# Performance work log

Measured on AMD Instinct MI355X. Metric: run time of the kernel, lower is better.

Reference implementation:

```python
import jax, jax.numpy as jnp
import numpy as np
from jax.scipy.special import logsumexp

T, N, M = 131072, 64, 8  # T_max, n_states, m_dimensions


def setup_inputs() -> dict:
    key = jax.random.key(0)
    k1, k2, k3, k4 = jax.random.split(key, 4)
    # observed Poisson counts, shape (T, M)
    x = jax.random.randint(k1, (T, M), 0, 20, dtype=jnp.int32)
    # Poisson rates per state/dimension (positive), shape (N, M)
    lambdas = jnp.exp(jax.random.uniform(k2, (N, M), dtype=jnp.float32) * 3.0)
    # column-stochastic transition matrix in log domain (softmax over dim 0, as in torch code)
    log_transition = jax.nn.log_softmax(
        jax.random.uniform(k3, (N, N), dtype=jnp.float32) * 10.0, axis=0)
    # log state priors, shape (N,)
    log_state_priors = jax.nn.log_softmax(
        jax.random.normal(k4, (N,), dtype=jnp.float32), axis=0)
    return {"x": x, "lambdas": lambdas, "log_transition": log_transition,
            "log_state_priors": log_state_priors}


def reference(x, lambdas, log_transition, log_state_priors):
    """log p(x) for a Poisson-emission HMM (forward algorithm in log domain)."""
    xf = x.astype(jnp.float32)                      # (T, M)
    log_lam = jnp.log(lambdas)                      # (N, M)
    # Poisson log-prob summed over dims: em[t,s] = sum_m x[t,m]*log lam[s,m] - lam[s,m] - lgamma(x[t,m]+1)
    log_em = (xf @ log_lam.T                        # (T, N)
              - lambdas.sum(axis=1)[None, :]
              - jax.lax.lgamma(xf + 1.0).sum(axis=1)[:, None])

    alpha0 = log_em[0] + log_state_priors           # (N,)

    def step(alpha_prev, em_t):
        # alpha[t,i] = em[t,i] + logsumexp_k (A[i,k] + alpha[t-1,k])
        alpha = em_t + logsumexp(log_transition + alpha_prev[None, :], axis=1)
        return alpha, None

    alpha_T, _ = jax.lax.scan(step, alpha0, log_em[1:])
    return logsumexp(alpha_T)
```

## Files before the change

### kernel.cpp

```cpp
#include <hip/hip_runtime.h>
#include <stdint.h>

#define TT 131072
#define MD 8
#define CHUNK 32
#define RMP 72

using f32x4  = __attribute__((ext_vector_type(4))) float;
using bf16x8 = __attribute__((ext_vector_type(8))) __bf16;
using bf16x2 = __attribute__((ext_vector_type(2))) __bf16;
using u32x2  = __attribute__((ext_vector_type(2))) uint32_t;
using u32x4  = __attribute__((ext_vector_type(4))) uint32_t;

__device__ __constant__ float c_lg[20] = {
    0.0f, 0.0f, 0.69314718f, 1.79175947f, 3.17805383f,
    4.78749174f, 6.57925121f, 8.52516136f, 10.60460290f, 12.80182748f,
    15.10441257f, 17.50230785f, 19.98721386f, 22.55216385f, 25.19122118f,
    27.89927138f, 30.67186011f, 33.50507345f, 36.39544521f, 39.33988419f};

#define MFMA(a, b, c) __builtin_amdgcn_mfma_f32_16x16x32_bf16((a), (b), (c), 0, 0, 0)

__device__ __forceinline__ uint32_t pk2(float lo, float hi) {
    bf16x2 t = {(__bf16)lo, (__bf16)hi};
    return __builtin_bit_cast(uint32_t, t);
}

__device__ __forceinline__ float wave_max_dpp(float v) {
    int x = __builtin_bit_cast(int, v);
#define DHOP(ctrl)                                                            \
    {                                                                         \
        int y = __builtin_amdgcn_update_dpp(x, x, ctrl, 0xf, 0xf, false);     \
        x = __builtin_bit_cast(int, fmaxf(__builtin_bit_cast(float, x),       \
                                          __builtin_bit_cast(float, y)));     \
    }
    DHOP(0x111)
    DHOP(0x112)
    DHOP(0x114)
    DHOP(0x118)
    DHOP(0x142)
    DHOP(0x143)
#undef DHOP
    return __builtin_bit_cast(float, __builtin_amdgcn_readlane(x, 63));
}


__device__ __forceinline__ void emis(const int4& xa, const int4& xb,
                                     const float* ll, float lamsum,
                                     const float* lgt, float& pe, float& gs) {
    float g = -lamsum;
    g = fmaf((float)xa.x, ll[0], g);
    g = fmaf((float)xa.y, ll[1], g);
    g = fmaf((float)xa.z, ll[2], g);
    g = fmaf((float)xa.w, ll[3], g);
    g = fmaf((float)xb.x, ll[4], g);
    g = fmaf((float)xb.y, ll[5], g);
    g = fmaf((float)xb.z, ll[6], g);
    g = fmaf((float)xb.w, ll[7], g);
    float Lt = lgt[xa.x] + lgt[xa.y] + lgt[xa.z] + lgt[xa.w] +
               lgt[xb.x] + lgt[xb.y] + lgt[xb.z] + lgt[xb.w];
    float gm = wave_max_dpp(g);
    pe = __expf(g - gm);
    gs = gm - Lt;
}

__device__ __forceinline__ void emis_ng(const int4& xa, const int4& xb,
                                        const float* ll, float lamsum,
                                        float& pe, float& gm_out) {
    float g = -lamsum;
    g = fmaf((float)xa.x, ll[0], g);
    g = fmaf((float)xa.y, ll[1], g);
    g = fmaf((float)xa.z, ll[2], g);
    g = fmaf((float)xa.w, ll[3], g);
    g = fmaf((float)xb.x, ll[4], g);
    g = fmaf((float)xb.y, ll[5], g);
    g = fmaf((float)xb.z, ll[6], g);
    g = fmaf((float)xb.w, ll[7], g);
    float gm = wave_max_dpp(g);
    pe = __expf(g - gm);
    gm_out = gm;
}


__device__ __forceinline__ void identity_B(bf16x8 B[2][4], int li, int q) {
#pragma unroll
    for (int kf = 0; kf < 2; ++kf)
#pragma unroll
        for (int nb = 0; nb < 4; ++nb) {
            int n = 16 * nb + li;
            u32x4 u;
#pragma unroll
            for (int wi = 0; wi < 4; ++wi) {
                int k0 = 32 * kf + 16 * (wi >> 1) + 4 * q + 2 * (wi & 1);
                uint32_t v = 0;
                if (k0 == n) v |= 0x3F80u;
                if (k0 + 1 == n) v |= 0x3F800000u;
                u[wi] = v;
            }
            B[kf][nb] = __builtin_bit_cast(bf16x8, u);
        }
}

__device__ __forceinline__ void state_to_rm(short* rm, const bf16x8 B[2][4],
                                            int li, int q) {
#pragma unroll
    for (int kf = 0; kf < 2; ++kf)
#pragma unroll
        for (int nb = 0; nb < 4; ++nb) {
            u32x4 u = __builtin_bit_cast(u32x4, B[kf][nb]);
            int n = 16 * nb + li;
#pragma unroll
            for (int wi = 0; wi < 4; ++wi) {
                int k0 = 32 * kf + 16 * (wi >> 1) + 4 * q + 2 * (wi & 1);
                uint32_t v = u[wi];
                rm[k0 * RMP + n] = (short)(v & 0xFFFFu);
                rm[(k0 + 1) * RMP + n] = (short)(v >> 16);
            }
        }
}

__device__ __forceinline__ void dump_rm_g(short* gm, const bf16x8 B[2][4],
                                          int li, int q) {
#pragma unroll
    for (int kf = 0; kf < 2; ++kf)
#pragma unroll
        for (int nb = 0; nb < 4; ++nb) {
            u32x4 u = __builtin_bit_cast(u32x4, B[kf][nb]);
            int n = 16 * nb + li;
#pragma unroll
            for (int wi = 0; wi < 4; ++wi) {
                int k0 = 32 * kf + 16 * (wi >> 1) + 4 * q + 2 * (wi & 1);
                uint32_t v = u[wi];
                gm[k0 * 64 + n] = (short)(v & 0xFFFFu);
                gm[(k0 + 1) * 64 + n] = (short)(v >> 16);
            }
        }
}

__device__ __forceinline__ void load_afrags(const short* rm, int li, int q,
                                            bf16x8 A[4][2]) {
#pragma unroll
    for (int mb = 0; mb < 4; ++mb)
#pragma unroll
        for (int kf = 0; kf < 2; ++kf) {
            const short* p = rm + (16 * mb + li) * RMP + 32 * kf + 4 * q;
            u32x2 lo = *(const u32x2*)p;
            u32x2 hi = *(const u32x2*)(p + 16);
            u32x4 u = {lo[0], lo[1], hi[0], hi[1]};
            A[mb][kf] = __builtin_bit_cast(bf16x8, u);
        }
}

__device__ __forceinline__ void load_afrags_g(const short* gm, int li, int q,
                                              bf16x8 A[4][2]) {
#pragma unroll
    for (int mb = 0; mb < 4; ++mb)
#pragma unroll
        for (int kf = 0; kf < 2; ++kf) {
            const short* p = gm + (16 * mb + li) * 64 + 32 * kf + 4 * q;
            u32x2 lo = *(const u32x2*)p;
            u32x2 hi = *(const u32x2*)(p + 16);
            u32x4 u = {lo[0], lo[1], hi[0], hi[1]};
            A[mb][kf] = __builtin_bit_cast(bf16x8, u);
        }
}

__device__ __forceinline__ float leftmul(const bf16x8 A[4][2], bf16x8 B[2][4]) {
    f32x4 d[4][4];
#pragma unroll
    for (int mb = 0; mb < 4; ++mb)
#pragma unroll
        for (int nb = 0; nb < 4; ++nb) {
            f32x4 z = {0.f, 0.f, 0.f, 0.f};
            d[mb][nb] = MFMA(A[mb][0], B[0][nb], z);
            d[mb][nb] = MFMA(A[mb][1], B[1][nb], d[mb][nb]);
        }
    float pm = 0.f;
#pragma unroll
    for (int mb = 0; mb < 4; ++mb)
#pragma unroll
        for (int nb = 0; nb < 4; ++nb)
            pm = fmaxf(pm, fmaxf(fmaxf(d[mb][nb][0], d[mb][nb][1]),
                                 fmaxf(d[mb][nb][2], d[mb][nb][3])));
    pm = wave_max_dpp(pm);
    pm = fmaxf(pm, 1e-30f);
    float r = 1.0f / pm;
#pragma unroll
    for (int mb = 0; mb < 4; ++mb)
#pragma unroll
        for (int nb = 0; nb < 4; ++nb) {
#pragma unroll
            for (int reg = 0; reg < 4; ++reg)
                B[mb >> 1][nb][(mb & 1) * 4 + reg] =
                    (__bf16)(d[mb][nb][reg] * r);
        }
    return pm;
}

#define STEPE(BIN, BOUT, NRM, GSC, GSN, SACC, CHI)                           \
    {                                                                        \
        int sl_ = s + 2 > CHUNK - 1 ? CHUNK - 1 : s + 2;                     \
        int4 xa_ = xs[w][CHI * 64 + 2 * sl_];                                \
        int4 xb_ = xs[w][CHI * 64 + 2 * sl_ + 1];                            \
        float pen_, gmn_;                                                    \
        emis_ng(xa_, xb_, ll, lamsum, pen_, gmn_);                           \
        GSN = gmn_;                                                          \
        pes[(s + 2) & 3][CHI][w][l] = pen_;                                  \
        float r_ = 1.0f / NRM;                                               \
        SACC += (double)GSC + (double)__logf(NRM);                           \
        const float* pc_ = &pes[s & 3][CHI][w][0];                           \
        f32x4 scv0 = *(const f32x4*)(pc_ + 4 * q) * r_;                      \
        f32x4 scv1 = *(const f32x4*)(pc_ + 16 + 4 * q) * r_;                 \
        f32x4 scv2 = *(const f32x4*)(pc_ + 32 + 4 * q) * r_;                 \
        f32x4 scv3 = *(const f32x4*)(pc_ + 48 + 4 * q) * r_;                 \
        f32x4 mx_ = {0.f, 0.f, 0.f, 0.f};                                    \
        _Pragma("unroll") for (int nb = 0; nb < 4; ++nb) {                   \
            f32x4 z = {0.f, 0.f, 0.f, 0.f};                                  \
            f32x4 d0 = MFMA(TA[0][0], BIN[0][nb], z);                        \
            d0 = MFMA(TA[0][1], BIN[1][nb], d0);                             \
            f32x4 d1 = MFMA(TA[1][0], BIN[0][nb], z);                        \
            d1 = MFMA(TA[1][1], BIN[1][nb], d1);                             \
            d0 *= scv0;                                                      \
            d1 *= scv1;                                                      \
            mx_ = __builtin_elementwise_max(mx_, d0);                        \
            mx_ = __builtin_elementwise_max(mx_, d1);                        \
            u32x4 u0 = {pk2(d0[0], d0[1]), pk2(d0[2], d0[3]),                \
                        pk2(d1[0], d1[1]), pk2(d1[2], d1[3])};               \
            BOUT[0][nb] = __builtin_bit_cast(bf16x8, u0);                    \
            f32x4 d2 = MFMA(TA[2][0], BIN[0][nb], z);                        \
            d2 = MFMA(TA[2][1], BIN[1][nb], d2);                             \
            f32x4 d3 = MFMA(TA[3][0], BIN[0][nb], z);                        \
            d3 = MFMA(TA[3][1], BIN[1][nb], d3);                             \
            d2 *= scv2;                                                      \
            d3 *= scv3;                                                      \
            mx_ = __builtin_elementwise_max(mx_, d2);                        \
            mx_ = __builtin_elementwise_max(mx_, d3);                        \
            u32x4 u1 = {pk2(d2[0], d2[1]), pk2(d2[2], d2[3]),                \
                        pk2(d3[0], d3[1]), pk2(d3[2], d3[3])};               \
            BOUT[1][nb] = __builtin_bit_cast(bf16x8, u1);                    \
        }                                                                    \
        float pm_ = fmaxf(fmaxf(mx_[0], mx_[1]), fmaxf(mx_[2], mx_[3]));     \
        pm_ = wave_max_dpp(pm_);                                             \
        NRM = fmaxf(pm_, 1e-30f);                                            \
    }

#define STEPO(BIN, BOUT, GSC, GSN, SACC, CHI)                                \
    {                                                                        \
        int sl_ = s + 2 > CHUNK - 1 ? CHUNK - 1 : s + 2;                     \
        int4 xa_ = xs[w][CHI * 64 + 2 * sl_];                                \
        int4 xb_ = xs[w][CHI * 64 + 2 * sl_ + 1];                            \
        float pen_, gmn_;                                                    \
        emis_ng(xa_, xb_, ll, lamsum, pen_, gmn_);                           \
        GSN = gmn_;                                                          \
        pes[(s + 2) & 3][CHI][w][l] = pen_;                                  \
        SACC += (double)GSC;                                                 \
        const float* pc_ = &pes[s & 3][CHI][w][0];                           \
        f32x4 scv0 = *(const f32x4*)(pc_ + 4 * q);                           \
        f32x4 scv1 = *(const f32x4*)(pc_ + 16 + 4 * q);                      \
        f32x4 scv2 = *(const f32x4*)(pc_ + 32 + 4 * q);                      \
        f32x4 scv3 = *(const f32x4*)(pc_ + 48 + 4 * q);                      \
        _Pragma("unroll") for (int nb = 0; nb < 4; ++nb) {                   \
            f32x4 z = {0.f, 0.f, 0.f, 0.f};                                  \
            f32x4 d0 = MFMA(TA[0][0], BIN[0][nb], z);                        \
            d0 = MFMA(TA[0][1], BIN[1][nb], d0);                             \
            f32x4 d1 = MFMA(TA[1][0], BIN[0][nb], z);                        \
            d1 = MFMA(TA[1][1], BIN[1][nb], d1);                             \
            d0 *= scv0;                                                      \
            d1 *= scv1;                                                      \
            u32x4 u0 = {pk2(d0[0], d0[1]), pk2(d0[2], d0[3]),                \
                        pk2(d1[0], d1[1]), pk2(d1[2], d1[3])};               \
            BOUT[0][nb] = __builtin_bit_cast(bf16x8, u0);                    \
            f32x4 d2 = MFMA(TA[2][0], BIN[0][nb], z);                        \
            d2 = MFMA(TA[2][1], BIN[1][nb], d2);                             \
            f32x4 d3 = MFMA(TA[3][0], BIN[0][nb], z);                        \
            d3 = MFMA(TA[3][1], BIN[1][nb], d3);                             \
            d2 *= scv2;                                                      \
            d3 *= scv3;                                                      \
            u32x4 u1 = {pk2(d2[0], d2[1]), pk2(d2[2], d2[3]),                \
                        pk2(d3[0], d3[1]), pk2(d3[2], d3[3])};               \
            BOUT[1][nb] = __builtin_bit_cast(bf16x8, u1);                    \
        }                                                                    \
        XAUNUSED                                                             \
    }
#define XAUNUSED

__global__ __launch_bounds__(256, 2) void k_chunks(
    const int* __restrict__ x, const float* __restrict__ lambdas,
    const float* __restrict__ logT, short* __restrict__ M1,
    double* __restrict__ S1) {
    __shared__ short rm[4][64 * RMP];
    __shared__ float pes[4][2][4][64];
    __shared__ int4 xs[4][128];
    __shared__ float lgt[20];
    __shared__ double Sw[4];
    const int tid = threadIdx.x;
    const int l = tid & 63, w = tid >> 6;
    const int li = l & 15, q = l >> 4;
    if (tid < 20) lgt[tid] = c_lg[tid];

    const int c0 = (blockIdx.x * 4 + w) * 2;
    const int t0a = 1 + c0 * CHUNK;
    const int t0b = t0a + CHUNK;
    const int lenB = min(CHUNK, TT - t0b);

    {
        int r0 = l >> 1, h = l & 1;
        int tr0 = t0a + r0;
        tr0 = tr0 > TT - 1 ? TT - 1 : tr0;
        xs[w][l] = *(const int4*)(x + (size_t)tr0 * MD + h * 4);
        int tr1 = t0a + 32 + r0;
        tr1 = tr1 > TT - 1 ? TT - 1 : tr1;
        xs[w][l + 64] = *(const int4*)(x + (size_t)tr1 * MD + h * 4);
    }

    float ll[8];
    float lamsum = 0.f;
#pragma unroll
    for (int m = 0; m < 8; ++m) {
        float lam = lambdas[l * 8 + m];
        ll[m] = __logf(lam);
        lamsum += lam;
    }

    bf16x8 TA[4][2];
#pragma unroll
    for (int mb = 0; mb < 4; ++mb)
#pragma unroll
        for (int kf = 0; kf < 2; ++kf) {
            const float* tp = logT + (16 * mb + li) * 64 + 32 * kf + 4 * q;
            float4 v0 = *(const float4*)tp;
            float4 v1 = *(const float4*)(tp + 16);
            bf16x8 a;
            a[0] = (__bf16)__expf(v0.x);
            a[1] = (__bf16)__expf(v0.y);
            a[2] = (__bf16)__expf(v0.z);
            a[3] = (__bf16)__expf(v0.w);
            a[4] = (__bf16)__expf(v1.x);
            a[5] = (__bf16)__expf(v1.y);
            a[6] = (__bf16)__expf(v1.z);
            a[7] = (__bf16)__expf(v1.w);
            TA[mb][kf] = a;
        }

    bf16x8 B0a[2][4], B1a[2][4], B0b[2][4], B1b[2][4];
    identity_B(B0a, li, q);
    identity_B(B0b, li, q);
    __syncthreads();

    double Sa = 0.0, Sb = 0.0;
    float nA_a = 1.0f, nA_b = 1.0f;
    float gE0a, gE1a, gO0a, gO1a;
    float gE0b, gE1b, gO0b, gO1b;
    {
        float pe_;
        emis_ng(xs[w][0], xs[w][1], ll, lamsum, pe_, gE0a);
        pes[0][0][w][l] = pe_;
        emis_ng(xs[w][2], xs[w][3], ll, lamsum, pe_, gO0a);
        pes[1][0][w][l] = pe_;
        emis_ng(xs[w][64], xs[w][65], ll, lamsum, pe_, gE0b);
        pes[0][1][w][l] = pe_;
        emis_ng(xs[w][66], xs[w][67], ll, lamsum, pe_, gO0b);
        pes[1][1][w][l] = pe_;
    }

    int s = 0;
#pragma unroll 1
    for (int p = 0; p < 7; ++p) {
        STEPE(B0a, B1a, nA_a, gE0a, gE1a, Sa, 0);
        STEPE(B0b, B1b, nA_b, gE0b, gE1b, Sb, 1);
        ++s;
        STEPO(B1a, B0a, gO0a, gO1a, Sa, 0);
        STEPO(B1b, B0b, gO0b, gO1b, Sb, 1);
        ++s;
        STEPE(B0a, B1a, nA_a, gE1a, gE0a, Sa, 0);
        STEPE(B0b, B1b, nA_b, gE1b, gE0b, Sb, 1);
        ++s;
        STEPO(B1a, B0a, gO1a, gO0a, Sa, 0);
        STEPO(B1b, B0b, gO1b, gO0b, Sb, 1);
        ++s;
    }
    STEPE(B0a, B1a, nA_a, gE0a, gE1a, Sa, 0);
    STEPE(B0b, B1b, nA_b, gE0b, gE1b, Sb, 1);
    ++s;
    STEPO(B1a, B0a, gO0a, gO1a, Sa, 0);
    STEPO(B1b, B0b, gO0b, gO1b, Sb, 1);
    ++s;
    STEPE(B0a, B1a, nA_a, gE1a, gE0a, Sa, 0);
    STEPE(B0b, B1b, nA_b, gE1b, gE0b, Sb, 1);
    ++s;
    STEPO(B1a, B0a, gO1a, gO0a, Sa, 0);
    if (lenB == CHUNK) {
        STEPO(B1b, B0b, gO1b, gO0b, Sb, 1);
    } else {
#pragma unroll
        for (int kf = 0; kf < 2; ++kf)
#pragma unroll
            for (int nb = 0; nb < 4; ++nb) B0b[kf][nb] = B1b[kf][nb];
    }

    {
        const int lenTot = CHUNK + lenB;
        float lt = 0.f;
        if (l < lenTot) {
            int4 a = xs[w][2 * l], b = xs[w][2 * l + 1];
            lt = lgt[a.x] + lgt[a.y] + lgt[a.z] + lgt[a.w] + lgt[b.x] +
                 lgt[b.y] + lgt[b.z] + lgt[b.w];
        }
#pragma unroll
        for (int m = 1; m <= 32; m <<= 1) lt += __shfl_xor(lt, m, 64);
        Sa -= (double)lt;
    }

    state_to_rm(&rm[w][0], B0b, li, q);
    {
        bf16x8 Ap[4][2];
        load_afrags(&rm[w][0], li, q, Ap);
        float pm = leftmul(Ap, B0a);
        Sa += Sb + (double)__logf(pm);
    }

    __syncthreads();
    if (w) state_to_rm(&rm[w][0], B0a, li, q);
    if (l == 0) Sw[w] = Sa;
    __syncthreads();
    if (w == 0) {
        double S = Sa;
#pragma unroll 1
        for (int j = 1; j < 4; ++j) {
            bf16x8 A[4][2];
            load_afrags(&rm[j][0], li, q, A);
            float pm = leftmul(A, B0a);
            S += Sw[j] + (double)__logf(pm);
        }
        dump_rm_g(M1 + (size_t)blockIdx.x * 4096, B0a, li, q);
        if (l == 0) S1[blockIdx.x] = S;
    }
}

__global__ __launch_bounds__(256, 1) void k_combine(
    const short* __restrict__ M1, const double* __restrict__ S1,
    short* __restrict__ M2, double* __restrict__ S2) {
    __shared__ short rm[4][64 * RMP];
    __shared__ double Sw[4];
    const int tid = threadIdx.x;
    const int l = tid & 63, w = tid >> 6;
    const int li = l & 15, q = l >> 4;
    const int base = (blockIdx.x * 4 + w) * 4;

    bf16x8 B[2][4];
    identity_B(B, li, q);
    double S = 0.0;
    bf16x8 Aa[4][2], Ab[4][2];
    load_afrags_g(M1 + (size_t)base * 4096, li, q, Aa);
    load_afrags_g(M1 + (size_t)(base + 1) * 4096, li, q, Ab);
    float pm = leftmul(Aa, B);
    S += S1[base] + (double)__logf(pm);
    load_afrags_g(M1 + (size_t)(base + 2) * 4096, li, q, Aa);
    pm = leftmul(Ab, B);
    S += S1[base + 1] + (double)__logf(pm);
    load_afrags_g(M1 + (size_t)(base + 3) * 4096, li, q, Ab);
    pm = leftmul(Aa, B);
    S += S1[base + 2] + (double)__logf(pm);
    pm = leftmul(Ab, B);
    S += S1[base + 3] + (double)__logf(pm);

    if (w) state_to_rm(&rm[w][0], B, li, q);
    if (l == 0) Sw[w] = S;
    __syncthreads();
    if (w == 0) {
#pragma unroll 1
        for (int j = 1; j < 4; ++j) {
            bf16x8 A[4][2];
            load_afrags(&rm[j][0], li, q, A);
            float pmj = leftmul(A, B);
            S += Sw[j] + (double)__logf(pmj);
        }
        dump_rm_g(M2 + (size_t)blockIdx.x * 4096, B, li, q);
        if (l == 0) S2[blockIdx.x] = S;
    }
}

__global__ __launch_bounds__(256, 1) void k_final(
    const int* __restrict__ x, const float* __restrict__ lambdas,
    const float* __restrict__ prior, const short* __restrict__ M2,
    const double* __restrict__ S2, float* __restrict__ out) {
    __shared__ short rm[4][64 * RMP];
    __shared__ double Sw[4];
    __shared__ float lgt[20];
    const int tid = threadIdx.x;
    const int l = tid & 63, w = tid >> 6;
    const int li = l & 15, q = l >> 4;
    if (tid < 20) lgt[tid] = c_lg[tid];
    __syncthreads();

    const int base = w * 8;
    bf16x8 B[2][4];
    identity_B(B, li, q);
    double S = 0.0;
    bf16x8 Aa[4][2], Ab[4][2];
    load_afrags_g(M2 + (size_t)base * 4096, li, q, Aa);
#pragma unroll
    for (int j = 0; j < 8; j += 2) {
        load_afrags_g(M2 + (size_t)(base + j + 1) * 4096, li, q, Ab);
        float pm = leftmul(Aa, B);
        S += S2[base + j] + (double)__logf(pm);
        if (j + 2 < 8)
            load_afrags_g(M2 + (size_t)(base + j + 2) * 4096, li, q, Aa);
        pm = leftmul(Ab, B);
        S += S2[base + j + 1] + (double)__logf(pm);
    }

    if (w) state_to_rm(&rm[w][0], B, li, q);
    if (l == 0) Sw[w] = S;
    __syncthreads();
    if (w == 0) {
#pragma unroll 1
        for (int j = 1; j < 4; ++j) {
            bf16x8 A[4][2];
            load_afrags(&rm[j][0], li, q, A);
            float pm = leftmul(A, B);
            S += Sw[j] + (double)__logf(pm);
        }
        float ll[8];
        float lamsum = 0.f;
#pragma unroll
        for (int m = 0; m < 8; ++m) {
            float lam = lambdas[l * 8 + m];
            ll[m] = __logf(lam);
            lamsum += lam;
        }
        int4 xa = *(const int4*)(x);
        int4 xb = *(const int4*)(x + 4);
        float pe0, gs0;
        emis(xa, xb, ll, lamsum, lgt, pe0, gs0);
        S += (double)gs0;
        float a0 = pe0 * __expf(prior[l]);

        float av[4];
#pragma unroll
        for (int nb = 0; nb < 4; ++nb) av[nb] = __shfl(a0, 16 * nb + li, 64);

        float acc = 0.f;
#pragma unroll
        for (int kf = 0; kf < 2; ++kf)
#pragma unroll
            for (int nb = 0; nb < 4; ++nb) {
                u32x4 u = __builtin_bit_cast(u32x4, B[kf][nb]);
#pragma unroll
                for (int e = 0; e < 4; ++e) {
                    float flo = __builtin_bit_cast(float, u[e] << 16);
                    float fhi = __builtin_bit_cast(float, u[e] & 0xFFFF0000u);
                    acc = fmaf(flo + fhi, av[nb], acc);
                }
            }
#pragma unroll
        for (int m = 1; m <= 32; m <<= 1) acc += __shfl_xor(acc, m, 64);
        if (l == 0) out[0] = (float)(S + (double)__logf(acc));
    }
}

extern "C" void kernel_launch(void* const* d_in, const int* in_sizes, int n_in,
                              void* d_out, int out_size, void* d_ws,
                              size_t ws_size, hipStream_t stream) {
    const int* x = (const int*)d_in[0];
    const float* lambdas = (const float*)d_in[1];
    const float* logT = (const float*)d_in[2];
    const float* prior = (const float*)d_in[3];
    float* out = (float*)d_out;
    char* ws = (char*)d_ws;
    short* M1 = (short*)ws;
    double* S1 = (double*)(ws + 4194304);
    short* M2 = (short*)(ws + 4198400);
    double* S2 = (double*)(ws + 4460544);

    k_chunks<<<512, 256, 0, stream>>>(x, lambdas, logT, M1, S1);
    k_combine<<<32, 256, 0, stream>>>(M1, S1, M2, S2);
    k_final<<<1, 256, 0, stream>>>(x, lambdas, prior, M2, S2, out);
}
```

Baseline: 115.1 us.

## Halve chunk length, alias scratch onto rm LDS, double chunk-level parallelism

```diff
diff --git a/kernel.cpp b/kernel.cpp
--- a/kernel.cpp
+++ b/kernel.cpp
@@ -3,7 +3,7 @@
 
 #define TT 131072
 #define MD 8
-#define CHUNK 32
+#define CHUNK 16
 #define RMP 72
 
 using f32x4  = __attribute__((ext_vector_type(4))) float;
@@ -199,15 +199,15 @@
 #define STEPE(BIN, BOUT, NRM, GSC, GSN, SACC, CHI)                           \
     {                                                                        \
         int sl_ = s + 2 > CHUNK - 1 ? CHUNK - 1 : s + 2;                     \
-        int4 xa_ = xs[w][CHI * 64 + 2 * sl_];                                \
-        int4 xb_ = xs[w][CHI * 64 + 2 * sl_ + 1];                            \
+        int4 xa_ = xw[CHI * 32 + 2 * sl_];                                   \
+        int4 xb_ = xw[CHI * 32 + 2 * sl_ + 1];                               \
         float pen_, gmn_;                                                    \
         emis_ng(xa_, xb_, ll, lamsum, pen_, gmn_);                           \
         GSN = gmn_;                                                          \
-        pes[(s + 2) & 3][CHI][w][l] = pen_;                                  \
+        pesf[(((s + 2) & 3) * 8 + CHI * 4 + w) * 64 + l] = pen_;             \
         float r_ = 1.0f / NRM;                                               \
         SACC += (double)GSC + (double)__logf(NRM);                           \
-        const float* pc_ = &pes[s & 3][CHI][w][0];                           \
+        const float* pc_ = pesf + ((s & 3) * 8 + CHI * 4 + w) * 64;          \
         f32x4 scv0 = *(const f32x4*)(pc_ + 4 * q) * r_;                      \
         f32x4 scv1 = *(const f32x4*)(pc_ + 16 + 4 * q) * r_;                 \
         f32x4 scv2 = *(const f32x4*)(pc_ + 32 + 4 * q) * r_;                 \
@@ -246,14 +246,14 @@
 #define STEPO(BIN, BOUT, GSC, GSN, SACC, CHI)                                \
     {                                                                        \
         int sl_ = s + 2 > CHUNK - 1 ? CHUNK - 1 : s + 2;                     \
-        int4 xa_ = xs[w][CHI * 64 + 2 * sl_];                                \
-        int4 xb_ = xs[w][CHI * 64 + 2 * sl_ + 1];                            \
+        int4 xa_ = xw[CHI * 32 + 2 * sl_];                                   \
+        int4 xb_ = xw[CHI * 32 + 2 * sl_ + 1];                               \
         float pen_, gmn_;                                                    \
         emis_ng(xa_, xb_, ll, lamsum, pen_, gmn_);                           \
         GSN = gmn_;                                                          \
-        pes[(s + 2) & 3][CHI][w][l] = pen_;                                  \
+        pesf[(((s + 2) & 3) * 8 + CHI * 4 + w) * 64 + l] = pen_;             \
         SACC += (double)GSC;                                                 \
-        const float* pc_ = &pes[s & 3][CHI][w][0];                           \
+        const float* pc_ = pesf + ((s & 3) * 8 + CHI * 4 + w) * 64;          \
         f32x4 scv0 = *(const f32x4*)(pc_ + 4 * q);                           \
         f32x4 scv1 = *(const f32x4*)(pc_ + 16 + 4 * q);                      \
         f32x4 scv2 = *(const f32x4*)(pc_ + 32 + 4 * q);                      \
@@ -279,22 +279,21 @@
                         pk2(d3[0], d3[1]), pk2(d3[2], d3[3])};               \
             BOUT[1][nb] = __builtin_bit_cast(bf16x8, u1);                    \
         }                                                                    \
-        XAUNUSED                                                             \
-    }
-#define XAUNUSED
-
-__global__ __launch_bounds__(256, 2) void k_chunks(
+    }
+
+__global__ __launch_bounds__(256, 4) void k_chunks(
     const int* __restrict__ x, const float* __restrict__ lambdas,
     const float* __restrict__ logT, short* __restrict__ M1,
     double* __restrict__ S1) {
     __shared__ short rm[4][64 * RMP];
-    __shared__ float pes[4][2][4][64];
-    __shared__ int4 xs[4][128];
     __shared__ float lgt[20];
     __shared__ double Sw[4];
+    float* const pesf = (float*)&rm[0][0];
+    int4* const xsb = (int4*)((char*)&rm[0][0] + 8192);
     const int tid = threadIdx.x;
     const int l = tid & 63, w = tid >> 6;
     const int li = l & 15, q = l >> 4;
+    const int4* const xw = xsb + w * 64;
     if (tid < 20) lgt[tid] = c_lg[tid];
 
     const int c0 = (blockIdx.x * 4 + w) * 2;
@@ -304,12 +303,9 @@
 
     {
         int r0 = l >> 1, h = l & 1;
-        int tr0 = t0a + r0;
-        tr0 = tr0 > TT - 1 ? TT - 1 : tr0;
-        xs[w][l] = *(const int4*)(x + (size_t)tr0 * MD + h * 4);
-        int tr1 = t0a + 32 + r0;
-        tr1 = tr1 > TT - 1 ? TT - 1 : tr1;
-        xs[w][l + 64] = *(const int4*)(x + (size_t)tr1 * MD + h * 4);
+        int tr = t0a + r0;
+        tr = tr > TT - 1 ? TT - 1 : tr;
+        xsb[w * 64 + l] = *(const int4*)(x + (size_t)tr * MD + h * 4);
     }
 
     float ll[8];
@@ -352,19 +348,19 @@
     float gE0b, gE1b, gO0b, gO1b;
     {
         float pe_;
-        emis_ng(xs[w][0], xs[w][1], ll, lamsum, pe_, gE0a);
-        pes[0][0][w][l] = pe_;
-        emis_ng(xs[w][2], xs[w][3], ll, lamsum, pe_, gO0a);
-        pes[1][0][w][l] = pe_;
-        emis_ng(xs[w][64], xs[w][65], ll, lamsum, pe_, gE0b);
-        pes[0][1][w][l] = pe_;
-        emis_ng(xs[w][66], xs[w][67], ll, lamsum, pe_, gO0b);
-        pes[1][1][w][l] = pe_;
+        emis_ng(xw[0], xw[1], ll, lamsum, pe_, gE0a);
+        pesf[(0 * 8 + 0 * 4 + w) * 64 + l] = pe_;
+        emis_ng(xw[2], xw[3], ll, lamsum, pe_, gO0a);
+        pesf[(1 * 8 + 0 * 4 + w) * 64 + l] = pe_;
+        emis_ng(xw[32], xw[33], ll, lamsum, pe_, gE0b);
+        pesf[(0 * 8 + 1 * 4 + w) * 64 + l] = pe_;
+        emis_ng(xw[34], xw[35], ll, lamsum, pe_, gO0b);
+        pesf[(1 * 8 + 1 * 4 + w) * 64 + l] = pe_;
     }
 
     int s = 0;
 #pragma unroll 1
-    for (int p = 0; p < 7; ++p) {
+    for (int p = 0; p < 3; ++p) {
         STEPE(B0a, B1a, nA_a, gE0a, gE1a, Sa, 0);
         STEPE(B0b, B1b, nA_b, gE0b, gE1b, Sb, 1);
         ++s;
@@ -401,7 +397,7 @@
         const int lenTot = CHUNK + lenB;
         float lt = 0.f;
         if (l < lenTot) {
-            int4 a = xs[w][2 * l], b = xs[w][2 * l + 1];
+            int4 a = xw[2 * l], b = xw[2 * l + 1];
             lt = lgt[a.x] + lgt[a.y] + lgt[a.z] + lgt[a.w] + lgt[b.x] +
                  lgt[b.y] + lgt[b.z] + lgt[b.w];
         }
@@ -409,6 +405,7 @@
         for (int m = 1; m <= 32; m <<= 1) lt += __shfl_xor(lt, m, 64);
         Sa -= (double)lt;
     }
+    __syncthreads();
 
     state_to_rm(&rm[w][0], B0b, li, q);
     {
@@ -492,18 +489,18 @@
     if (tid < 20) lgt[tid] = c_lg[tid];
     __syncthreads();
 
-    const int base = w * 8;
+    const int base = w * 16;
     bf16x8 B[2][4];
     identity_B(B, li, q);
     double S = 0.0;
     bf16x8 Aa[4][2], Ab[4][2];
     load_afrags_g(M2 + (size_t)base * 4096, li, q, Aa);
 #pragma unroll
-    for (int j = 0; j < 8; j += 2) {
+    for (int j = 0; j < 16; j += 2) {
         load_afrags_g(M2 + (size_t)(base + j + 1) * 4096, li, q, Ab);
         float pm = leftmul(Aa, B);
         S += S2[base + j] + (double)__logf(pm);
-        if (j + 2 < 8)
+        if (j + 2 < 16)
             load_afrags_g(M2 + (size_t)(base + j + 2) * 4096, li, q, Aa);
         pm = leftmul(Ab, B);
         S += S2[base + j + 1] + (double)__logf(pm);
@@ -568,11 +565,11 @@
     float* out = (float*)d_out;
     char* ws = (char*)d_ws;
     short* M1 = (short*)ws;
-    double* S1 = (double*)(ws + 4194304);
-    short* M2 = (short*)(ws + 4198400);
-    double* S2 = (double*)(ws + 4460544);
-
-    k_chunks<<<512, 256, 0, stream>>>(x, lambdas, logT, M1, S1);
-    k_combine<<<32, 256, 0, stream>>>(M1, S1, M2, S2);
+    double* S1 = (double*)(ws + 8388608);
+    short* M2 = (short*)(ws + 8396800);
+    double* S2 = (double*)(ws + 8921088);
+
+    k_chunks<<<1024, 256, 0, stream>>>(x, lambdas, logT, M1, S1);
+    k_combine<<<64, 256, 0, stream>>>(M1, S1, M2, S2);
     k_final<<<1, 256, 0, stream>>>(x, lambdas, prior, M2, S2, out);
 }
```

New measurement: 305.1 us. 165% more time.
